# Kernel tuning notes

Hardware: AMD Instinct MI355X
Metric: run time of the kernel (lower is better)

## Reference

```python
import jax, jax.numpy as jnp
import numpy as np
import math

B, S, D, H, DK, FF, L = 4, 1024, 512, 8, 64, 2048, 4
IN, NS, SD, TOPK = 768, 4, 64, 2


def _ln(x, g, b, eps=1e-5):
    mu = jnp.mean(x, -1, keepdims=True)
    var = jnp.mean((x - mu) ** 2, -1, keepdims=True)
    return (x - mu) / jnp.sqrt(var + eps) * g + b


def _pos_emb(s, d):
    pos = jnp.arange(s, dtype=jnp.float32)[:, None]
    div = jnp.exp(jnp.arange(0, d, 2, dtype=jnp.float32) * (-math.log(10000.0) / d))
    pe = jnp.zeros((s, d), jnp.float32)
    pe = pe.at[:, 0::2].set(jnp.sin(pos * div))
    pe = pe.at[:, 1::2].set(jnp.cos(pos * div))
    return pe


def setup_inputs() -> dict:
    key = jax.random.key(0)
    ks = iter(jax.random.split(key, 40))
    r = lambda *sh: jax.random.normal(next(ks), sh, jnp.float32)
    p = lambda *sh: jax.random.normal(next(ks), sh, jnp.float32) * 0.02
    inp = {
        'q_raw_seq': r(B, S, NS, IN),
        'm_seq': r(B, S, SD),
        'qa_embed': r(B, S, D),
        # MoE expert FFNs: Linear(IN,IN) -> ReLU -> Linear(IN,D)
        'exp_w1': p(NS, IN, IN), 'exp_b1': jnp.zeros((NS, IN)),
        'exp_w2': p(NS, IN, D), 'exp_b2': jnp.zeros((NS, D)),
        # router input adapter Linear(NS*IN, D)
        'adapt_w': p(NS * IN, D), 'adapt_b': jnp.zeros((D,)),
        'gate_w': p(D + SD, NS), 'gate_b': jnp.zeros((NS,)),
        'moe_ln_g': jnp.ones((D,)), 'moe_ln_b': jnp.zeros((D,)),
        # transformer blocks (kq_same=1 -> k_linear shared for q and k)
        'kw': p(L, D, D), 'kb': jnp.zeros((L, D)),
        'vw': p(L, D, D), 'vb': jnp.zeros((L, D)),
        'ow': p(L, D, D), 'ob': jnp.zeros((L, D)),
        'ln1_g': jnp.ones((L, D)), 'ln1_b': jnp.zeros((L, D)),
        'ff_w1': p(L, D, FF), 'ff_b1': jnp.zeros((L, FF)),
        'ff_w2': p(L, FF, D), 'ff_b2': jnp.zeros((L, D)),
        'ln2_g': jnp.ones((L, D)), 'ln2_b': jnp.zeros((L, D)),
    }
    return inp


def _forward(q_raw_seq, m_seq, qa_embed, exp_w1, exp_b1, exp_w2, exp_b2,
             adapt_w, adapt_b, gate_w, gate_b, moe_ln_g, moe_ln_b,
             kw, kb, vw, vb, ow, ob, ln1_g, ln1_b,
             ff_w1, ff_b1, ff_w2, ff_b2, ln2_g, ln2_b):
    # ---- PolyaParallelMoE (eval: no noise/dropout), has_stages=True ----
    h1 = jax.nn.relu(jnp.einsum('bske,kef->bskf', q_raw_seq, exp_w1) + exp_b1[None, None])
    experts = jnp.einsum('bskf,kfm->bskm', h1, exp_w2) + exp_b2[None, None]  # [B,S,4,D]
    q_flat = q_raw_seq.reshape(q_raw_seq.shape[0], q_raw_seq.shape[1], NS * IN)
    summary = jax.nn.relu(q_flat @ adapt_w + adapt_b)
    logits = jnp.concatenate([summary, m_seq], -1) @ gate_w + gate_b  # [B,S,4]
    top_vals, _ = jax.lax.top_k(logits, TOPK)
    thresh = top_vals[..., -1:]
    masked = jnp.where(logits >= thresh, logits, -jnp.inf)  # scatter top-k, -inf elsewhere
    gate_weights = jax.nn.softmax(masked, -1)
    combined = jnp.einsum('bskm,bsk->bsm', experts, gate_weights)
    q_embed = _ln(combined, moe_ln_g, moe_ln_b)

    # ---- Architecture: positional add + causal transformer blocks ----
    pe = _pos_emb(S, D)
    x = q_embed + pe
    y = qa_embed + pe
    allow = jnp.tril(jnp.ones((S, S), bool), -1)  # strict lower: np.triu(k=0)==0
    scale = 1.0 / math.sqrt(DK)
    for i in range(L):
        kh = (x @ kw[i] + kb[i]).reshape(B, S, H, DK).transpose(0, 2, 1, 3)
        vh = (y @ vw[i] + vb[i]).reshape(B, S, H, DK).transpose(0, 2, 1, 3)
        # kq_same: q = k_linear(query), query==key==x -> qh == kh
        scores = jnp.einsum('bhid,bhjd->bhij', kh, kh) * scale
        scores = jnp.where(allow, scores, -1e32)
        attn = jax.nn.softmax(scores, -1)
        attn = attn.at[:, :, 0, :].set(0.0)  # zero_pad first query row
        ctx = jnp.einsum('bhij,bhjd->bhid', attn, vh).transpose(0, 2, 1, 3).reshape(B, S, D)
        x = _ln(x + (ctx @ ow[i] + ob[i]), ln1_g[i], ln1_b[i])
        ffn = jax.nn.relu(x @ ff_w1[i] + ff_b1[i]) @ ff_w2[i] + ff_b2[i]
        x = _ln(x + ffn, ln2_g[i], ln2_b[i])
        y = x  # after first block, value stream follows torch loop (values=y fixed)
        y = qa_embed + pe  # values stay qa stream per Architecture.forward
    return x


def reference(q_raw_seq, m_seq, qa_embed, exp_w1, exp_b1, exp_w2, exp_b2,
              adapt_w, adapt_b, gate_w, gate_b, moe_ln_g, moe_ln_b,
              kw, kb, vw, vb, ow, ob, ln1_g, ln1_b,
              ff_w1, ff_b1, ff_w2, ff_b2, ln2_g, ln2_b):
    # NOTE: in Architecture.forward, each block is called with query=x, key=x, values=y
    # where y = qa_embed + pe stays fixed across blocks.
    def fwd(*a):
        return _forward(*a)
    return fwd(q_raw_seq, m_seq, qa_embed, exp_w1, exp_b1, exp_w2, exp_b2,
               adapt_w, adapt_b, gate_w, gate_b, moe_ln_g, moe_ln_b,
               kw, kb, vw, vb, ow, ob, ln1_g, ln1_b,
               ff_w1, ff_b1, ff_w2, ff_b2, ln2_g, ln2_b)
```

## Files before the change

kernel.cpp:

```cpp
#include <hip/hip_runtime.h>
#include <hip/hip_bf16.h>

typedef unsigned short u16;
typedef __attribute__((ext_vector_type(8))) short short8;
typedef __attribute__((ext_vector_type(4))) float floatx4;

template <typename T> struct is_u16 { static constexpr bool v = false; };
template <> struct is_u16<u16> { static constexpr bool v = true; };

__device__ __forceinline__ float bf2f(u16 u) {
    unsigned x = (unsigned)u << 16;
    return __uint_as_float(x);
}
__device__ __forceinline__ u16 f2bf(float f) {
    unsigned x = __float_as_uint(f);
    unsigned r = (x + 0x7fffu + ((x >> 16) & 1u)) >> 16;
    return (u16)r;
}

__device__ __forceinline__ float wave_sum(float v) {
    #pragma unroll
    for (int off = 32; off; off >>= 1) v += __shfl_xor(v, off);
    return v;
}

__device__ __forceinline__ void async16(const u16* g, const u16* lds) {
    __builtin_amdgcn_global_load_lds(
        (const __attribute__((address_space(1))) void*)g,
        (__attribute__((address_space(3))) void*)lds, 16, 0, 0);
}

__device__ __forceinline__ void load8f(const float* p, u16* dst) {
    float4 a = *(const float4*)p, b = *(const float4*)(p + 4);
    dst[0] = f2bf(a.x); dst[1] = f2bf(a.y); dst[2] = f2bf(a.z); dst[3] = f2bf(a.w);
    dst[4] = f2bf(b.x); dst[5] = f2bf(b.y); dst[6] = f2bf(b.z); dst[7] = f2bf(b.w);
}

__device__ __forceinline__ void hilo8(const float* p, u16* hi, u16* lo) {
    float4 a = *(const float4*)p, b = *(const float4*)(p + 4);
    float v[8] = {a.x, a.y, a.z, a.w, b.x, b.y, b.z, b.w};
    #pragma unroll
    for (int i = 0; i < 8; ++i) {
        u16 h = f2bf(v[i]);
        hi[i] = h;
        lo[i] = f2bf(v[i] - bf2f(h));
    }
}

template <typename TA>
__device__ __forceinline__ void gemm_body(
    const TA* __restrict__ A, int lda,
    const u16* __restrict__ Bt, int ldb,
    const float* __restrict__ bias,
    float* __restrict__ Cf, u16* __restrict__ Cb, int ldc,
    int K, int act, int transC)
{
    __shared__ __align__(16) u16 Asm[128 * 32];
    __shared__ __align__(16) u16 Bsm[128 * 32];

    const int tid = threadIdx.x;
    const int lane = tid & 63;
    const int wave = tid >> 6;
    const int m0 = blockIdx.y * 128, n0 = blockIdx.x * 128;
    const int wm = (wave >> 1) * 64, wn = (wave & 1) * 64;

    const int r0 = tid >> 2;
    const int kc = (tid & 3) * 8;

    const int kq = (lane >> 4) * 8;
    const int fm = lane & 15;

    const floatx4 zz = {0.f, 0.f, 0.f, 0.f};
    floatx4 acc[4][4];
    #pragma unroll
    for (int mt = 0; mt < 4; ++mt)
        #pragma unroll
        for (int nt = 0; nt < 4; ++nt) acc[mt][nt] = zz;

    const u16* ldsA0 = Asm + wave * 512;
    const u16* ldsA1 = Asm + 2048 + wave * 512;
    const u16* ldsB0 = Bsm + wave * 512;
    const u16* ldsB1 = Bsm + 2048 + wave * 512;

    for (int kt = 0; kt < K; kt += 32) {
        if constexpr (is_u16<TA>::v) {
            async16(&A[(size_t)(m0 + r0) * lda + kt + kc],      ldsA0);
            async16(&A[(size_t)(m0 + r0 + 64) * lda + kt + kc], ldsA1);
            async16(&Bt[(size_t)(n0 + r0) * ldb + kt + kc],      ldsB0);
            async16(&Bt[(size_t)(n0 + r0 + 64) * ldb + kt + kc], ldsB1);
        } else {
            load8f(&A[(size_t)(m0 + r0) * lda + kt + kc],      &Asm[r0 * 32 + kc]);
            load8f(&A[(size_t)(m0 + r0 + 64) * lda + kt + kc], &Asm[(r0 + 64) * 32 + kc]);
            *(uint4*)&Bsm[r0 * 32 + kc]        = *(const uint4*)&Bt[(size_t)(n0 + r0) * ldb + kt + kc];
            *(uint4*)&Bsm[(r0 + 64) * 32 + kc] = *(const uint4*)&Bt[(size_t)(n0 + r0 + 64) * ldb + kt + kc];
        }
        __syncthreads();

        short8 af[4], bfr[4];
        #pragma unroll
        for (int mt = 0; mt < 4; ++mt)
            af[mt] = *(const short8*)&Asm[(wm + mt * 16 + fm) * 32 + kq];
        #pragma unroll
        for (int nt = 0; nt < 4; ++nt)
            bfr[nt] = *(const short8*)&Bsm[(wn + nt * 16 + fm) * 32 + kq];

        #pragma unroll
        for (int mt = 0; mt < 4; ++mt)
            #pragma unroll
            for (int nt = 0; nt < 4; ++nt)
                acc[mt][nt] = __builtin_amdgcn_mfma_f32_16x16x32_bf16(
                    af[mt], bfr[nt], acc[mt][nt], 0, 0, 0);
        __syncthreads();
    }

    const int cr = (lane >> 4) * 4;
    #pragma unroll
    for (int mt = 0; mt < 4; ++mt) {
        #pragma unroll
        for (int nt = 0; nt < 4; ++nt) {
            const int col = n0 + wn + nt * 16 + fm;
            const float bz = bias ? bias[col] : 0.f;
            #pragma unroll
            for (int r = 0; r < 4; ++r) {
                const int row = m0 + wm + mt * 16 + cr + r;
                float v = acc[mt][nt][r] + bz;
                if (act) v = fmaxf(v, 0.f);
                if (Cf) Cf[(size_t)row * ldc + col] = v;
                if (Cb) {
                    if (transC)
                        Cb[(((size_t)(row >> 10) * 512 + col) << 10) + (row & 1023)] = f2bf(v);
                    else
                        Cb[(size_t)row * ldc + col] = f2bf(v);
                }
            }
        }
    }
}

template <typename TA>
__global__ __launch_bounds__(256) void gemm_bf16(
    const TA* __restrict__ A, int lda, long strideAz,
    const u16* __restrict__ Bt, int ldb, long strideBz,
    const float* __restrict__ bias, int strideBiasZ,
    float* __restrict__ Cf, u16* __restrict__ Cb, int ldc, long strideCz,
    int K, int act, int transC)
{
    A += (size_t)blockIdx.z * strideAz;
    Bt += (size_t)blockIdx.z * strideBz;
    if (bias) bias += (size_t)blockIdx.z * strideBiasZ;
    if (Cf) Cf += (size_t)blockIdx.z * strideCz;
    if (Cb) Cb += (size_t)blockIdx.z * strideCz;
    gemm_body<TA>(A, lda, Bt, ldb, bias, Cf, Cb, ldc, K, act, transC);
}

__global__ __launch_bounds__(256) void gemm_kv(
    const u16* __restrict__ xb, const u16* __restrict__ yb,
    const u16* __restrict__ kwt, const u16* __restrict__ vwt,
    const float* __restrict__ kb, const float* __restrict__ vb,
    u16* __restrict__ khb, u16* __restrict__ vhT)
{
    if (blockIdx.z == 0)
        gemm_body<u16>(xb, 512, kwt, 512, kb, nullptr, khb, 512, 512, 0, 0);
    else
        gemm_body<u16>(yb, 512, vwt, 512, vb, nullptr, vhT, 512, 512, 0, 1);
}

__global__ __launch_bounds__(256) void gemm_f32split(
    const float* __restrict__ A, int lda,
    const u16* __restrict__ Bh, const u16* __restrict__ Bl, int ldb,
    float* __restrict__ Cf, int ldc, long strideCz,
    int kz)
{
    __shared__ __align__(16) u16 Ahs[64 * 32];
    __shared__ __align__(16) u16 Als[64 * 32];
    __shared__ __align__(16) u16 Bhs[128 * 32];
    __shared__ __align__(16) u16 Bls[128 * 32];

    const int tid = threadIdx.x;
    const int lane = tid & 63;
    const int wave = tid >> 6;
    const int m0 = blockIdx.y * 64, n0 = blockIdx.x * 128;
    const int wm = (wave >> 1) * 32, wn = (wave & 1) * 64;
    const int k0 = blockIdx.z * kz;
    Cf += (size_t)blockIdx.z * strideCz;

    const int r0 = tid >> 2;
    const int kc = (tid & 3) * 8;
    const int kq = (lane >> 4) * 8;
    const int fm = lane & 15;

    const floatx4 zz = {0.f, 0.f, 0.f, 0.f};
    floatx4 acc[2][4];
    #pragma unroll
    for (int mt = 0; mt < 2; ++mt)
        #pragma unroll
        for (int nt = 0; nt < 4; ++nt) acc[mt][nt] = zz;

    const u16* ldsB0h = Bhs + wave * 512;
    const u16* ldsB1h = Bhs + 2048 + wave * 512;
    const u16* ldsB0l = Bls + wave * 512;
    const u16* ldsB1l = Bls + 2048 + wave * 512;

    for (int kt = 0; kt < kz; kt += 32) {
        hilo8(&A[(size_t)(m0 + r0) * lda + k0 + kt + kc],
              &Ahs[r0 * 32 + kc], &Als[r0 * 32 + kc]);
        async16(&Bh[(size_t)(n0 + r0) * ldb + k0 + kt + kc],      ldsB0h);
        async16(&Bh[(size_t)(n0 + r0 + 64) * ldb + k0 + kt + kc], ldsB1h);
        async16(&Bl[(size_t)(n0 + r0) * ldb + k0 + kt + kc],      ldsB0l);
        async16(&Bl[(size_t)(n0 + r0 + 64) * ldb + k0 + kt + kc], ldsB1l);
        __syncthreads();

        short8 ah[2], al[2], bh[4], bl[4];
        #pragma unroll
        for (int mt = 0; mt < 2; ++mt) {
            ah[mt] = *(const short8*)&Ahs[(wm + mt * 16 + fm) * 32 + kq];
            al[mt] = *(const short8*)&Als[(wm + mt * 16 + fm) * 32 + kq];
        }
        #pragma unroll
        for (int nt = 0; nt < 4; ++nt) {
            bh[nt] = *(const short8*)&Bhs[(wn + nt * 16 + fm) * 32 + kq];
            bl[nt] = *(const short8*)&Bls[(wn + nt * 16 + fm) * 32 + kq];
        }

        #pragma unroll
        for (int mt = 0; mt < 2; ++mt)
            #pragma unroll
            for (int nt = 0; nt < 4; ++nt) {
                acc[mt][nt] = __builtin_amdgcn_mfma_f32_16x16x32_bf16(
                    ah[mt], bh[nt], acc[mt][nt], 0, 0, 0);
                acc[mt][nt] = __builtin_amdgcn_mfma_f32_16x16x32_bf16(
                    al[mt], bh[nt], acc[mt][nt], 0, 0, 0);
                acc[mt][nt] = __builtin_amdgcn_mfma_f32_16x16x32_bf16(
                    ah[mt], bl[nt], acc[mt][nt], 0, 0, 0);
            }
        __syncthreads();
    }

    const int cr = (lane >> 4) * 4;
    #pragma unroll
    for (int mt = 0; mt < 2; ++mt) {
        #pragma unroll
        for (int nt = 0; nt < 4; ++nt) {
            const int col = n0 + wn + nt * 16 + fm;
            #pragma unroll
            for (int r = 0; r < 4; ++r) {
                const int row = m0 + wm + mt * 16 + cr + r;
                Cf[(size_t)row * ldc + col] = acc[mt][nt][r];
            }
        }
    }
}

__global__ __launch_bounds__(64) void gate_fused_kernel(
    const float* __restrict__ ps, const float* __restrict__ adapt_b,
    const float* __restrict__ m_seq,
    const float* __restrict__ gw, const float* __restrict__ gb,
    float* __restrict__ gates)
{
    const int r = blockIdx.x, t = threadIdx.x;
    float p0 = 0.f, p1 = 0.f, p2 = 0.f, p3 = 0.f;
    const float* pr = ps + (size_t)r * 512;
    for (int j = t; j < 512; j += 64) {
        float v = pr[j] + pr[j + 2097152] + pr[j + 4194304] + pr[j + 6291456] + adapt_b[j];
        float s = fmaxf(v, 0.f);
        const float* g = gw + (size_t)j * 4;
        p0 += s * g[0]; p1 += s * g[1]; p2 += s * g[2]; p3 += s * g[3];
    }
    {
        float m = m_seq[(size_t)r * 64 + t];
        const float* g = gw + (size_t)(512 + t) * 4;
        p0 += m * g[0]; p1 += m * g[1]; p2 += m * g[2]; p3 += m * g[3];
    }
    p0 = wave_sum(p0); p1 = wave_sum(p1); p2 = wave_sum(p2); p3 = wave_sum(p3);
    if (t == 0) {
        float lg[4] = { p0 + gb[0], p1 + gb[1], p2 + gb[2], p3 + gb[3] };
        float m1 = -INFINITY, m2 = -INFINITY;
        #pragma unroll
        for (int k = 0; k < 4; ++k) {
            float v = lg[k];
            if (v > m1) { m2 = m1; m1 = v; }
            else if (v > m2) { m2 = v; }
        }
        float wv[4], s = 0.f;
        #pragma unroll
        for (int k = 0; k < 4; ++k) {
            wv[k] = (lg[k] >= m2) ? __expf(lg[k] - m1) : 0.f;
            s += wv[k];
        }
        float inv = 1.f / s;
        #pragma unroll
        for (int k = 0; k < 4; ++k) gates[(size_t)r * 4 + k] = wv[k] * inv;
    }
}

__global__ __launch_bounds__(256) void tconv_kernel(
    const float* __restrict__ in, u16* __restrict__ out, int K, int N)
{
    __shared__ float t[32][33];
    const int n0 = blockIdx.x * 32, k0 = blockIdx.y * 32;
    const size_t bo = (size_t)blockIdx.z * K * N;
    const int tx = threadIdx.x & 31, ty = threadIdx.x >> 5;
    const float* src = in + bo;
    u16* dst = out + bo;
    #pragma unroll
    for (int r = ty; r < 32; r += 8) t[r][tx] = src[(size_t)(k0 + r) * N + n0 + tx];
    __syncthreads();
    #pragma unroll
    for (int r = ty; r < 32; r += 8) dst[(size_t)(n0 + r) * K + k0 + tx] = f2bf(t[tx][r]);
}

__global__ __launch_bounds__(256) void tconv_hilo_kernel(
    const float* __restrict__ in, u16* __restrict__ outh, u16* __restrict__ outl,
    int K, int N)
{
    __shared__ float t[32][33];
    const int n0 = blockIdx.x * 32, k0 = blockIdx.y * 32;
    const int tx = threadIdx.x & 31, ty = threadIdx.x >> 5;
    #pragma unroll
    for (int r = ty; r < 32; r += 8) t[r][tx] = in[(size_t)(k0 + r) * N + n0 + tx];
    __syncthreads();
    #pragma unroll
    for (int r = ty; r < 32; r += 8) {
        float v = t[tx][r];
        u16 h = f2bf(v);
        outh[(size_t)(n0 + r) * K + k0 + tx] = h;
        outl[(size_t)(n0 + r) * K + k0 + tx] = f2bf(v - bf2f(h));
    }
}

__global__ void pe_kernel(float* __restrict__ pe)
{
    int idx = blockIdx.x * 256 + threadIdx.x;
    int s = idx >> 9, d = idx & 511;
    float div = expf((float)(d & ~1) * (-9.210340371976184f / 512.0f));
    float ang = (float)s * div;
    pe[idx] = (d & 1) ? cosf(ang) : sinf(ang);
}

__global__ void y_kernel(const float* __restrict__ qa, const float* __restrict__ pe,
                         u16* __restrict__ yb)
{
    int idx = blockIdx.x * 256 + threadIdx.x;
    yb[idx] = f2bf(qa[idx] + pe[idx & 524287]);
}

__global__ __launch_bounds__(64) void moe_ln_kernel(
    const u16* __restrict__ experts, const float* __restrict__ gates,
    const float* __restrict__ g, const float* __restrict__ bb,
    const float* __restrict__ pe, float* __restrict__ x, u16* __restrict__ xb)
{
    const int r = blockIdx.x, t = threadIdx.x;
    const u16* e = experts + (size_t)r * 2048;
    const float g0 = gates[r * 4 + 0], g1 = gates[r * 4 + 1];
    const float g2 = gates[r * 4 + 2], g3 = gates[r * 4 + 3];
    float v[8];
    #pragma unroll
    for (int it = 0; it < 8; ++it) {
        int d = t + it * 64;
        v[it] = g0 * bf2f(e[d]) + g1 * bf2f(e[512 + d])
              + g2 * bf2f(e[1024 + d]) + g3 * bf2f(e[1536 + d]);
    }
    float s = 0.f;
    #pragma unroll
    for (int it = 0; it < 8; ++it) s += v[it];
    s = wave_sum(s);
    const float mu = s * (1.f / 512.f);
    float q = 0.f;
    #pragma unroll
    for (int it = 0; it < 8; ++it) { float dd = v[it] - mu; q += dd * dd; }
    q = wave_sum(q);
    const float rstd = rsqrtf(q * (1.f / 512.f) + 1e-5f);
    const float* per = pe + (size_t)(r & 1023) * 512;
    #pragma unroll
    for (int it = 0; it < 8; ++it) {
        int d = t + it * 64;
        float o = (v[it] - mu) * rstd * g[d] + bb[d] + per[d];
        x[(size_t)r * 512 + d] = o;
        xb[(size_t)r * 512 + d] = f2bf(o);
    }
}

__global__ __launch_bounds__(64) void add_ln_kernel(
    float* __restrict__ x, u16* __restrict__ xb,
    const float* __restrict__ t0, const float* __restrict__ t1,
    const float* __restrict__ bias,
    const float* __restrict__ g, const float* __restrict__ bb,
    float* __restrict__ out2)
{
    const int r = blockIdx.x, t = threadIdx.x;
    float* xr = x + (size_t)r * 512;
    float v[8];
    #pragma unroll
    for (int it = 0; it < 8; ++it) {
        int d = t + it * 64;
        float tv = t0[(size_t)r * 512 + d];
        if (t1) tv += t1[(size_t)r * 512 + d];
        if (bias) tv += bias[d];
        v[it] = xr[d] + tv;
    }
    float s = 0.f;
    #pragma unroll
    for (int it = 0; it < 8; ++it) s += v[it];
    s = wave_sum(s);
    const float mu = s * (1.f / 512.f);
    float q = 0.f;
    #pragma unroll
    for (int it = 0; it < 8; ++it) { float dd = v[it] - mu; q += dd * dd; }
    q = wave_sum(q);
    const float rstd = rsqrtf(q * (1.f / 512.f) + 1e-5f);
    #pragma unroll
    for (int it = 0; it < 8; ++it) {
        int d = t + it * 64;
        float o = (v[it] - mu) * rstd * g[d] + bb[d];
        xr[d] = o;
        xb[(size_t)r * 512 + d] = f2bf(o);
        if (out2) out2[(size_t)r * 512 + d] = o;
    }
}

__global__ __launch_bounds__(256) void attn_kernel(
    const u16* __restrict__ kh, const u16* __restrict__ vhT,
    u16* __restrict__ ctx)
{
    __shared__ __align__(16) u16 Qs[64 * 64];
    __shared__ __align__(16) u16 Ks[64 * 64];
    __shared__ __align__(16) u16 Vt[64 * 72];
    __shared__ __align__(16) u16 Ps[64 * 72];

    const int tid = threadIdx.x;
    const int lane = tid & 63, wave = tid >> 6;
    const int quad = lane >> 4, fm = lane & 15;
    const int b = blockIdx.x, h = blockIdx.y;
    const int bz = blockIdx.z;
    const int it = (bz < 8) ? bz : (23 - bz);

    const u16* khb = kh + ((size_t)b * 1024) * 512 + h * 64;
    const u16* vtb = vhT + ((size_t)(b * 512 + h * 64)) * 1024;

    const int lj = tid >> 2;
    const int lc = tid & 3;

    {
        const u16* src = khb + (size_t)(it * 64 + lj) * 512 + lc * 16;
        *(uint4*)&Qs[lj * 64 + lc * 16]     = *(const uint4*)src;
        *(uint4*)&Qs[lj * 64 + lc * 16 + 8] = *(const uint4*)(src + 8);
    }

    const floatx4 zz = {0.f, 0.f, 0.f, 0.f};
    floatx4 o_acc[4];
    #pragma unroll
    for (int nt = 0; nt < 4; ++nt) o_acc[nt] = zz;
    float m_run[4] = { -INFINITY, -INFINITY, -INFINITY, -INFINITY };
    float l_run[4] = {};

    __syncthreads();

    for (int jt = 0; jt <= it; ++jt) {
        {
            const u16* ksrc = khb + (size_t)(jt * 64 + lj) * 512 + lc * 16;
            *(uint4*)&Ks[lj * 64 + lc * 16]     = *(const uint4*)ksrc;
            *(uint4*)&Ks[lj * 64 + lc * 16 + 8] = *(const uint4*)(ksrc + 8);
            const u16* vsrc = vtb + (size_t)lj * 1024 + jt * 64 + lc * 16;
            *(uint4*)&Vt[lj * 72 + lc * 16]     = *(const uint4*)vsrc;
            *(uint4*)&Vt[lj * 72 + lc * 16 + 8] = *(const uint4*)(vsrc + 8);
        }
        __syncthreads();

        floatx4 s_acc[4];
        #pragma unroll
        for (int nt = 0; nt < 4; ++nt) s_acc[nt] = zz;
        #pragma unroll
        for (int ks = 0; ks < 2; ++ks) {
            short8 af = *(const short8*)&Qs[(wave * 16 + fm) * 64 + ks * 32 + quad * 8];
            #pragma unroll
            for (int nt = 0; nt < 4; ++nt) {
                short8 bf = *(const short8*)&Ks[(nt * 16 + fm) * 64 + ks * 32 + quad * 8];
                s_acc[nt] = __builtin_amdgcn_mfma_f32_16x16x32_bf16(af, bf, s_acc[nt], 0, 0, 0);
            }
        }

        const bool diag = (jt == it);
        #pragma unroll
        for (int r = 0; r < 4; ++r) {
            const int rowi = wave * 16 + quad * 4 + r;
            float sv[4];
            #pragma unroll
            for (int nt = 0; nt < 4; ++nt) {
                float s = s_acc[nt][r] * 0.125f;
                if (diag && (nt * 16 + fm) >= rowi) s = -INFINITY;
                sv[nt] = s;
            }
            float mx = fmaxf(fmaxf(sv[0], sv[1]), fmaxf(sv[2], sv[3]));
            #pragma unroll
            for (int off = 1; off < 16; off <<= 1) mx = fmaxf(mx, __shfl_xor(mx, off));
            const float mn = fmaxf(m_run[r], mx);
            const float mfix = (mn == -INFINITY) ? 0.f : mn;
            const float alpha = (m_run[r] == -INFINITY) ? 0.f : __expf(m_run[r] - mn);
            m_run[r] = mn;
            float rs = 0.f;
            #pragma unroll
            for (int nt = 0; nt < 4; ++nt) {
                float p = __expf(sv[nt] - mfix);
                Ps[rowi * 72 + nt * 16 + fm] = f2bf(p);
                rs += p;
            }
            #pragma unroll
            for (int off = 1; off < 16; off <<= 1) rs += __shfl_xor(rs, off);
            l_run[r] = l_run[r] * alpha + rs;
            #pragma unroll
            for (int nt = 0; nt < 4; ++nt) o_acc[nt][r] *= alpha;
        }
        __syncthreads();

        #pragma unroll
        for (int ks = 0; ks < 2; ++ks) {
            short8 af = *(const short8*)&Ps[(wave * 16 + fm) * 72 + ks * 32 + quad * 8];
            #pragma unroll
            for (int nt = 0; nt < 4; ++nt) {
                short8 bf = *(const short8*)&Vt[(nt * 16 + fm) * 72 + ks * 32 + quad * 8];
                o_acc[nt] = __builtin_amdgcn_mfma_f32_16x16x32_bf16(af, bf, o_acc[nt], 0, 0, 0);
            }
        }
        __syncthreads();
    }

    u16* cb = ctx + ((size_t)b * 1024 + (size_t)it * 64 + wave * 16) * 512 + h * 64;
    #pragma unroll
    for (int r = 0; r < 4; ++r) {
        const int row = quad * 4 + r;
        const float inv = (l_run[r] > 0.f) ? 1.f / l_run[r] : 0.f;
        #pragma unroll
        for (int nt = 0; nt < 4; ++nt)
            cb[(size_t)row * 512 + nt * 16 + fm] = f2bf(o_acc[nt][r] * inv);
    }
}

extern "C" void kernel_launch(void* const* d_in, const int* in_sizes, int n_in,
                              void* d_out, int out_size, void* d_ws, size_t ws_size,
                              hipStream_t stream)
{
    const float* q_raw   = (const float*)d_in[0];
    const float* m_seq   = (const float*)d_in[1];
    const float* qa      = (const float*)d_in[2];
    const float* exp_w1  = (const float*)d_in[3];
    const float* exp_b1  = (const float*)d_in[4];
    const float* exp_w2  = (const float*)d_in[5];
    const float* exp_b2  = (const float*)d_in[6];
    const float* adapt_w = (const float*)d_in[7];
    const float* adapt_b = (const float*)d_in[8];
    const float* gate_w  = (const float*)d_in[9];
    const float* gate_b  = (const float*)d_in[10];
    const float* moe_g   = (const float*)d_in[11];
    const float* moe_b   = (const float*)d_in[12];
    const float* kw      = (const float*)d_in[13];
    const float* kb      = (const float*)d_in[14];
    const float* vw      = (const float*)d_in[15];
    const float* vb      = (const float*)d_in[16];
    const float* ow      = (const float*)d_in[17];
    const float* ob      = (const float*)d_in[18];
    const float* ln1g    = (const float*)d_in[19];
    const float* ln1b    = (const float*)d_in[20];
    const float* fw1     = (const float*)d_in[21];
    const float* fb1     = (const float*)d_in[22];
    const float* fw2     = (const float*)d_in[23];
    const float* fb2     = (const float*)d_in[24];
    const float* ln2g    = (const float*)d_in[25];
    const float* ln2b    = (const float*)d_in[26];
    float* out = (float*)d_out;

    const size_t NEED = 78708736ull;
    if (ws_size < NEED) return;

    char* base = (char*)d_ws;
    float* x  = (float*)(base + 0);
    u16*  xb  = (u16*)(base + 8388608);
    u16*  yb  = (u16*)(base + 12582912);
    char* G = base + 16777216;
    u16*   w1t     = (u16*)(G + 0);
    u16*   w2t     = (u16*)(G + 4718592);
    float* psum    = (float*)(G + 7864320);
    u16*   h1b4    = (u16*)(G + 7864320);
    u16*   expb    = (u16*)(G + 33030144);
    float* pe      = (float*)(G + 49807360);
    float* gates   = (float*)(G + 51904512);
    u16*   adwh    = (u16*)(G + 52428800);
    u16*   adwl    = (u16*)(G + 55574528);
    u16*   kwt  = (u16*)(G + 0);
    u16*   vwt  = (u16*)(G + 2097152);
    u16*   owt  = (u16*)(G + 4194304);
    u16*   fw1t = (u16*)(G + 6291456);
    u16*   fw2t = (u16*)(G + 14680064);
    u16*   khb  = (u16*)(G + 23068672);
    u16*   vhT  = (u16*)(G + 27262976);
    u16*   ctxb = (u16*)(G + 31457280);
    float* p    = (float*)(G + 35651584);
    u16*   ffhb = (u16*)(G + 44040192);
    float* ps0  = (float*)(G + 23068672);

    pe_kernel<<<2048, 256, 0, stream>>>(pe);
    tconv_kernel<<<dim3(24, 24, 4), 256, 0, stream>>>(exp_w1, w1t, 768, 768);
    tconv_kernel<<<dim3(16, 24, 4), 256, 0, stream>>>(exp_w2, w2t, 768, 512);
    tconv_hilo_kernel<<<dim3(16, 96), 256, 0, stream>>>(adapt_w, adwh, adwl, 3072, 512);

    gemm_f32split<<<dim3(4, 64, 4), 256, 0, stream>>>(
        q_raw, 3072, adwh, adwl, 3072, psum, 512, 2097152L, 768);
    gate_fused_kernel<<<4096, 64, 0, stream>>>(
        psum, adapt_b, m_seq, gate_w, gate_b, gates);

    gemm_bf16<float><<<dim3(6, 32, 4), 256, 0, stream>>>(
        q_raw, 3072, 768L, w1t, 768, 589824L, exp_b1, 768,
        nullptr, h1b4, 768, 3145728L, 768, 1, 0);
    gemm_bf16<u16><<<dim3(4, 32, 4), 256, 0, stream>>>(
        h1b4, 768, 3145728L, w2t, 768, 393216L, exp_b2, 512,
        nullptr, expb, 2048, 512L, 768, 0, 0);
    moe_ln_kernel<<<4096, 64, 0, stream>>>(expb, gates, moe_g, moe_b, pe, x, xb);
    y_kernel<<<8192, 256, 0, stream>>>(qa, pe, yb);

    tconv_kernel<<<dim3(16, 16, 4), 256, 0, stream>>>(kw, kwt, 512, 512);
    tconv_kernel<<<dim3(16, 16, 4), 256, 0, stream>>>(vw, vwt, 512, 512);
    tconv_kernel<<<dim3(16, 16, 4), 256, 0, stream>>>(ow, owt, 512, 512);
    tconv_kernel<<<dim3(64, 16, 4), 256, 0, stream>>>(fw1, fw1t, 512, 2048);
    tconv_kernel<<<dim3(16, 64, 4), 256, 0, stream>>>(fw2, fw2t, 2048, 512);

    for (int i = 0; i < 4; ++i) {
        gemm_kv<<<dim3(4, 32, 2), 256, 0, stream>>>(
            xb, yb, kwt + (size_t)i * 262144, vwt + (size_t)i * 262144,
            kb + i * 512, vb + i * 512, khb, vhT);
        attn_kernel<<<dim3(4, 8, 16), 256, 0, stream>>>(khb, vhT, ctxb);
        gemm_bf16<u16><<<dim3(4, 32), 256, 0, stream>>>(
            ctxb, 512, 0L, owt + (size_t)i * 262144, 512, 0L, ob + i * 512, 0,
            p, nullptr, 512, 0L, 512, 0, 0);
        add_ln_kernel<<<4096, 64, 0, stream>>>(
            x, xb, p, nullptr, nullptr, ln1g + i * 512, ln1b + i * 512, nullptr);
        gemm_bf16<u16><<<dim3(16, 32), 256, 0, stream>>>(
            xb, 512, 0L, fw1t + (size_t)i * 1048576, 512, 0L, fb1 + i * 2048, 0,
            nullptr, ffhb, 2048, 0L, 512, 1, 0);
        gemm_bf16<u16><<<dim3(4, 32, 2), 256, 0, stream>>>(
            ffhb, 2048, 1024L, fw2t + (size_t)i * 1048576, 2048, 1024L, nullptr, 0,
            ps0, nullptr, 512, 2097152L, 1024, 0, 0);
        add_ln_kernel<<<4096, 64, 0, stream>>>(
            x, xb, ps0, ps0 + 2097152, fb2 + i * 512,
            ln2g + i * 512, ln2b + i * 512, (i == 3) ? out : nullptr);
    }
}
```

Baseline: 971.2 us.

## Pre-split q_raw into bf16 hi/lo once and reuse across both GEMMs

```diff
diff --git a/kernel.cpp b/kernel.cpp
--- a/kernel.cpp
+++ b/kernel.cpp
@@ -45,6 +45,16 @@
         hi[i] = h;
         lo[i] = f2bf(v[i] - bf2f(h));
     }
+}
+
+__global__ __launch_bounds__(256) void hilo_conv_kernel(
+    const float* __restrict__ in, u16* __restrict__ hi, u16* __restrict__ lo)
+{
+    const size_t i = ((size_t)blockIdx.x * 256 + threadIdx.x) * 8;
+    u16 h[8], l[8];
+    hilo8(in + i, h, l);
+    *(uint4*)&hi[i] = *(const uint4*)h;
+    *(uint4*)&lo[i] = *(const uint4*)l;
 }
 
 template <typename TA>
@@ -166,21 +176,21 @@
 }
 
 __global__ __launch_bounds__(256) void gemm_f32split(
-    const float* __restrict__ A, int lda,
+    const u16* __restrict__ Ah, const u16* __restrict__ Al, int lda,
     const u16* __restrict__ Bh, const u16* __restrict__ Bl, int ldb,
     float* __restrict__ Cf, int ldc, long strideCz,
     int kz)
 {
-    __shared__ __align__(16) u16 Ahs[64 * 32];
-    __shared__ __align__(16) u16 Als[64 * 32];
+    __shared__ __align__(16) u16 Ahs[128 * 32];
+    __shared__ __align__(16) u16 Als[128 * 32];
     __shared__ __align__(16) u16 Bhs[128 * 32];
     __shared__ __align__(16) u16 Bls[128 * 32];
 
     const int tid = threadIdx.x;
     const int lane = tid & 63;
     const int wave = tid >> 6;
-    const int m0 = blockIdx.y * 64, n0 = blockIdx.x * 128;
-    const int wm = (wave >> 1) * 32, wn = (wave & 1) * 64;
+    const int m0 = blockIdx.y * 128, n0 = blockIdx.x * 128;
+    const int wm = (wave >> 1) * 64, wn = (wave & 1) * 64;
     const int k0 = blockIdx.z * kz;
     Cf += (size_t)blockIdx.z * strideCz;
 
@@ -190,29 +200,37 @@
     const int fm = lane & 15;
 
     const floatx4 zz = {0.f, 0.f, 0.f, 0.f};
-    floatx4 acc[2][4];
-    #pragma unroll
-    for (int mt = 0; mt < 2; ++mt)
+    floatx4 acc[4][4];
+    #pragma unroll
+    for (int mt = 0; mt < 4; ++mt)
         #pragma unroll
         for (int nt = 0; nt < 4; ++nt) acc[mt][nt] = zz;
 
-    const u16* ldsB0h = Bhs + wave * 512;
-    const u16* ldsB1h = Bhs + 2048 + wave * 512;
-    const u16* ldsB0l = Bls + wave * 512;
-    const u16* ldsB1l = Bls + 2048 + wave * 512;
+    const u16* ldsAh0 = Ahs + wave * 512;
+    const u16* ldsAh1 = Ahs + 2048 + wave * 512;
+    const u16* ldsAl0 = Als + wave * 512;
+    const u16* ldsAl1 = Als + 2048 + wave * 512;
+    const u16* ldsBh0 = Bhs + wave * 512;
+    const u16* ldsBh1 = Bhs + 2048 + wave * 512;
+    const u16* ldsBl0 = Bls + wave * 512;
+    const u16* ldsBl1 = Bls + 2048 + wave * 512;
 
     for (int kt = 0; kt < kz; kt += 32) {
-        hilo8(&A[(size_t)(m0 + r0) * lda + k0 + kt + kc],
-              &Ahs[r0 * 32 + kc], &Als[r0 * 32 + kc]);
-        async16(&Bh[(size_t)(n0 + r0) * ldb + k0 + kt + kc],      ldsB0h);
-        async16(&Bh[(size_t)(n0 + r0 + 64) * ldb + k0 + kt + kc], ldsB1h);
-        async16(&Bl[(size_t)(n0 + r0) * ldb + k0 + kt + kc],      ldsB0l);
-        async16(&Bl[(size_t)(n0 + r0 + 64) * ldb + k0 + kt + kc], ldsB1l);
+        const size_t ka = (size_t)(m0 + r0) * lda + k0 + kt + kc;
+        const size_t kb = (size_t)(n0 + r0) * ldb + k0 + kt + kc;
+        async16(&Ah[ka],                     ldsAh0);
+        async16(&Ah[ka + (size_t)64 * lda],  ldsAh1);
+        async16(&Al[ka],                     ldsAl0);
+        async16(&Al[ka + (size_t)64 * lda],  ldsAl1);
+        async16(&Bh[kb],                     ldsBh0);
+        async16(&Bh[kb + (size_t)64 * ldb],  ldsBh1);
+        async16(&Bl[kb],                     ldsBl0);
+        async16(&Bl[kb + (size_t)64 * ldb],  ldsBl1);
         __syncthreads();
 
-        short8 ah[2], al[2], bh[4], bl[4];
-        #pragma unroll
-        for (int mt = 0; mt < 2; ++mt) {
+        short8 ah[4], al[4], bh[4], bl[4];
+        #pragma unroll
+        for (int mt = 0; mt < 4; ++mt) {
             ah[mt] = *(const short8*)&Ahs[(wm + mt * 16 + fm) * 32 + kq];
             al[mt] = *(const short8*)&Als[(wm + mt * 16 + fm) * 32 + kq];
         }
@@ -223,7 +241,7 @@
         }
 
         #pragma unroll
-        for (int mt = 0; mt < 2; ++mt)
+        for (int mt = 0; mt < 4; ++mt)
             #pragma unroll
             for (int nt = 0; nt < 4; ++nt) {
                 acc[mt][nt] = __builtin_amdgcn_mfma_f32_16x16x32_bf16(
@@ -238,7 +256,7 @@
 
     const int cr = (lane >> 4) * 4;
     #pragma unroll
-    for (int mt = 0; mt < 2; ++mt) {
+    for (int mt = 0; mt < 4; ++mt) {
         #pragma unroll
         for (int nt = 0; nt < 4; ++nt) {
             const int col = n0 + wn + nt * 16 + fm;
@@ -568,7 +586,7 @@
     const float* ln2b    = (const float*)d_in[26];
     float* out = (float*)d_out;
 
-    const size_t NEED = 78708736ull;
+    const size_t NEED = 125829120ull;
     if (ws_size < NEED) return;
 
     char* base = (char*)d_ws;
@@ -585,6 +603,8 @@
     float* gates   = (float*)(G + 51904512);
     u16*   adwh    = (u16*)(G + 52428800);
     u16*   adwl    = (u16*)(G + 55574528);
+    u16*   qhi     = (u16*)(G + 58720256);
+    u16*   qlo     = (u16*)(G + 83886080);
     u16*   kwt  = (u16*)(G + 0);
     u16*   vwt  = (u16*)(G + 2097152);
     u16*   owt  = (u16*)(G + 4194304);
@@ -598,17 +618,18 @@
     float* ps0  = (float*)(G + 23068672);
 
     pe_kernel<<<2048, 256, 0, stream>>>(pe);
+    hilo_conv_kernel<<<6144, 256, 0, stream>>>(q_raw, qhi, qlo);
     tconv_kernel<<<dim3(24, 24, 4), 256, 0, stream>>>(exp_w1, w1t, 768, 768);
     tconv_kernel<<<dim3(16, 24, 4), 256, 0, stream>>>(exp_w2, w2t, 768, 512);
     tconv_hilo_kernel<<<dim3(16, 96), 256, 0, stream>>>(adapt_w, adwh, adwl, 3072, 512);
 
-    gemm_f32split<<<dim3(4, 64, 4), 256, 0, stream>>>(
-        q_raw, 3072, adwh, adwl, 3072, psum, 512, 2097152L, 768);
+    gemm_f32split<<<dim3(4, 32, 4), 256, 0, stream>>>(
+        qhi, qlo, 3072, adwh, adwl, 3072, psum, 512, 2097152L, 768);
     gate_fused_kernel<<<4096, 64, 0, stream>>>(
         psum, adapt_b, m_seq, gate_w, gate_b, gates);
 
-    gemm_bf16<float><<<dim3(6, 32, 4), 256, 0, stream>>>(
-        q_raw, 3072, 768L, w1t, 768, 589824L, exp_b1, 768,
+    gemm_bf16<u16><<<dim3(6, 32, 4), 256, 0, stream>>>(
+        qhi, 3072, 768L, w1t, 768, 589824L, exp_b1, 768,
         nullptr, h1b4, 768, 3145728L, 768, 1, 0);
     gemm_bf16<u16><<<dim3(4, 32, 4), 256, 0, stream>>>(
         h1b4, 768, 3145728L, w2t, 768, 393216L, exp_b2, 512,
```

Result: no change. 954.1 us (-1.8%).
